# Performance work log

Measured on AMD Instinct MI355X. Metric: run time of the kernel, lower is better.

The kernel has to match this reference:

```python
import jax, jax.numpy as jnp
import numpy as np

B = 131072    # batch of toy 2D points
H = 256       # effective hidden width (dims[1], = out_dims * group_card)
NB = 8        # n_blocks i-ResBlocks
NMID = 3      # middle layers: dims 2->256->256->256->256->2 => 1 in + 3 mid + 1 out
NPS = 5       # n_power_series terms for log-det trace estimator


def setup_inputs() -> dict:
    key = jax.random.key(0)
    ks = jax.random.split(key, 8)
    # small scales keep each g-net contractive (coeff<1 Lipschitz, as spectral norm would)
    x  = jax.random.normal(ks[0], (B, 2), jnp.float32)
    v  = jax.random.normal(ks[1], (B, 2), jnp.float32)  # Hutchinson probe (n_samples=1)
    Wi = jax.random.normal(ks[2], (NB, 2, H), jnp.float32) * 0.05
    bi = jax.random.normal(ks[3], (NB, H), jnp.float32) * 0.01
    Wm = jax.random.normal(ks[4], (NB, NMID, H, H), jnp.float32) * (0.05 / np.sqrt(H))
    bm = jax.random.normal(ks[5], (NB, NMID, H), jnp.float32) * 0.01
    Wo = jax.random.normal(ks[6], (NB, H, 2), jnp.float32) * (0.05 / np.sqrt(H))
    bo = jax.random.normal(ks[7], (NB, 2), jnp.float32) * 0.01
    return {"x": x, "v": v, "Wi": Wi, "bi": bi, "Wm": Wm, "bm": bm, "Wo": Wo, "bo": bo}


def _g(x, Wi, bi, Wm, bm, Wo, bo):
    # equivariant 3x3 convs on 1x1 spatial maps == channel-mixing linears;
    # build_nnet appends the activation after EVERY conv, including the last.
    h = jax.nn.relu(x @ Wi + bi)
    for j in range(Wm.shape[0]):
        h = jax.nn.relu(h @ Wm[j] + bm[j])
    return jax.nn.relu(h @ Wo + bo)


def _iresblock(x, v, Wi, bi, Wm, bm, Wo, bo):
    gfun = lambda xx: _g(xx, Wi, bi, Wm, bm, Wo, bo)
    gx = gfun(x)
    # log det(I + J_g) ~= sum_{k=1..n} (-1)^{k+1}/k * v^T J_g^k v  (power series, Hutchinson)
    w = v
    logdet = jnp.zeros((x.shape[0], 1), x.dtype)
    for k in range(1, NPS + 1):
        _, w = jax.jvp(gfun, (x,), (w,))          # w <- J_g @ w
        coef = ((-1.0) ** (k + 1)) / k
        logdet = logdet + coef * jnp.sum(w * v, axis=1, keepdims=True)
    return x + gx, logdet


def reference(x, v, Wi, bi, Wm, bm, Wo, bo):
    z = x
    delta_logp = jnp.zeros((x.shape[0], 1), x.dtype)  # SequentialFlow: logpx - logdet per block
    for b in range(NB):
        z, ld = _iresblock(z, v, Wi[b], bi[b], Wm[b], bm[b], Wo[b], bo[b])
        delta_logp = delta_logp - ld
    return z, delta_logp
```

## Files before the change

### kernel.cpp

```cpp
#include <hip/hip_runtime.h>
#include <hip/hip_bf16.h>

#define BATCH 131072
#define H 256
#define NBLK 8
#define NMID 3
#define MS 32
#define RT_N 6
#define NT 512

typedef __attribute__((ext_vector_type(8))) short short8;
typedef __attribute__((ext_vector_type(4))) float f32x4;

__device__ __forceinline__ unsigned pk2(float a, float b) {
    unsigned ua = __float_as_uint(a) + 0x8000u;
    unsigned ub = __float_as_uint(b) + 0x8000u;
    return __builtin_amdgcn_perm(ub, ua, 0x07060302u);
}

__global__ void pack_w_kernel(const float* __restrict__ Wm, unsigned short* __restrict__ Wp) {
    int o = blockIdx.x * blockDim.x + threadIdx.x;
    if (o >= NBLK * NMID * 8192) return;
    int lane  = o & 63;
    int T     = (o >> 6) & 15;
    int kk    = (o >> 10) & 7;
    int layer = o >> 13;
    int n  = (T >> 2) * 64 + (lane & 15) * 4 + (T & 3);
    int k0 = kk * 32 + (lane >> 4) * 8;
    const float* src = Wm + (size_t)layer * H * H;
    unsigned int w[4];
    #pragma unroll
    for (int jj = 0; jj < 4; ++jj)
        w[jj] = pk2(src[(size_t)(k0 + 2*jj) * H + n], src[(size_t)(k0 + 2*jj + 1) * H + n]);
    uint4 val; val.x = w[0]; val.y = w[1]; val.z = w[2]; val.w = w[3];
    ((uint4*)Wp)[o] = val;
}

__device__ __forceinline__ void epilogue_write(const f32x4 (&acc)[3][4],
                                               const float* __restrict__ bias,
                                               unsigned short* __restrict__ Xs,
                                               int rg, int cg, int lane) {
    const int mcol = lane & 15, quad = lane >> 4;
    const int nb = cg * 64 + mcol * 4;
    const float4 bv = *(const float4*)(bias + nb);
    const int kkx = nb >> 5;
    const int qx  = (nb >> 3) & 3;
    const int jb  = nb & 7;
    const int kx1 = kkx & 1;
    #pragma unroll
    for (int r = 0; r < 4; ++r) {
        float pre[4], hv[4], ta[4], tb[4];
        pre[0] = acc[0][0][r] + bv.x; pre[1] = acc[0][1][r] + bv.y;
        pre[2] = acc[0][2][r] + bv.z; pre[3] = acc[0][3][r] + bv.w;
        #pragma unroll
        for (int c = 0; c < 4; ++c) {
            bool mk = pre[c] > 0.0f;
            hv[c] = mk ? pre[c]      : 0.0f;
            ta[c] = mk ? acc[1][c][r] : 0.0f;
            tb[c] = mk ? acc[2][c][r] : 0.0f;
        }
        int rowm = quad * 4 + r;
        int le   = qx * 16 + rowm;
        int scl  = (le ^ ((le >> 3) & 7)) ^ kx1;
        int e0   = (((rg * 8 + kkx) * 64 + scl) * 8) + jb;
        uint2 ph; ph.x = pk2(hv[0], hv[1]); ph.y = pk2(hv[2], hv[3]);
        uint2 pa; pa.x = pk2(ta[0], ta[1]); pa.y = pk2(ta[2], ta[3]);
        uint2 pb; pb.x = pk2(tb[0], tb[1]); pb.y = pk2(tb[2], tb[3]);
        *(uint2*)(Xs + e0)          = ph;
        *(uint2*)(Xs + e0 + 8192)   = pa;
        *(uint2*)(Xs + e0 + 16384)  = pb;
    }
}

__global__ __launch_bounds__(NT, 4)
void flow_kernel(const float* __restrict__ x, const float* __restrict__ v,
                 const float* __restrict__ Wi, const float* __restrict__ bi,
                 const float* __restrict__ bm, const float* __restrict__ Wo,
                 const float* __restrict__ bo,
                 const unsigned short* __restrict__ Wp,
                 float* __restrict__ out)
{
    __shared__ uint4 Xl4[RT_N * 8 * 64];
    __shared__ float zbuf[MS * 2];
    __shared__ float vbuf[MS * 2];

    unsigned short* Xs = (unsigned short*)Xl4;

    const int tid  = threadIdx.x;
    const int wave = tid >> 6;
    const int lane = tid & 63;
    const int mcol = lane & 15;
    const int quad = lane >> 4;
    const int rg   = wave >> 2;
    const int cg   = wave & 3;
    const int s0   = blockIdx.x * MS;
    const int rl   = lane ^ ((lane >> 3) & 7);

    float dlp = 0.0f;
    if (tid < MS) {
        zbuf[tid*2+0] = x[(size_t)(s0+tid)*2+0];
        zbuf[tid*2+1] = x[(size_t)(s0+tid)*2+1];
        vbuf[tid*2+0] = v[(size_t)(s0+tid)*2+0];
        vbuf[tid*2+1] = v[(size_t)(s0+tid)*2+1];
    }
    __syncthreads();

    for (int b = 0; b < NBLK; ++b) {
        if (tid < 384) {
            int rt = tid >> 6, cl = tid & 63;
            int l = cl ^ ((cl >> 3) & 7);
            int m = l & 15, q = l >> 4;
            int st = rt >> 1;
            uint4 pk = {0u, 0u, 0u, 0u};
            if (q == 0) {
                if (st == 0) {
                    int s = ((rt & 1) << 4) | m;
                    pk.x = pk2(zbuf[s*2+0], zbuf[s*2+1]);
                } else if (st == 1) pk.x = 0x00003F80u;
                else                pk.x = 0x3F800000u;
            }
            Xl4[rt * 512 + cl] = pk;
        }
        __syncthreads();

        const float* Wi0 = Wi + (size_t)b * 2 * H;
        const float* Wi1 = Wi0 + H;
        {
            short8 b0f[4];
            #pragma unroll
            for (int ct = 0; ct < 4; ++ct) {
                short8 z = {0,0,0,0,0,0,0,0};
                if (lane < 16) {
                    int n = cg * 64 + lane * 4 + ct;
                    unsigned p = pk2(Wi0[n], Wi1[n]);
                    z[0] = (short)(p & 0xFFFFu);
                    z[1] = (short)(p >> 16);
                }
                b0f[ct] = z;
            }
            f32x4 acc[3][4];
            #pragma unroll
            for (int st = 0; st < 3; ++st)
                #pragma unroll
                for (int ct = 0; ct < 4; ++ct)
                    acc[st][ct] = (f32x4){0.f, 0.f, 0.f, 0.f};
            #pragma unroll
            for (int st = 0; st < 3; ++st) {
                int rt = st * 2 + rg;
                short8 af = ((const short8*)Xl4)[(rt * 8) * 64 + rl];
                #pragma unroll
                for (int ct = 0; ct < 4; ++ct)
                    acc[st][ct] = __builtin_amdgcn_mfma_f32_16x16x32_bf16(af, b0f[ct], acc[st][ct], 0, 0, 0);
            }
            __syncthreads();
            epilogue_write(acc, bi + (size_t)b * H, Xs, rg, cg, lane);
            __syncthreads();
        }

        for (int li = 0; li < NMID; ++li) {
            const int layer = b * NMID + li;
            const short8* Bp  = ((const short8*)Wp) + (size_t)layer * 8192;
            const float* bias = bm + (size_t)layer * H;

            f32x4 acc[3][4];
            #pragma unroll
            for (int st = 0; st < 3; ++st)
                #pragma unroll
                for (int ct = 0; ct < 4; ++ct)
                    acc[st][ct] = (f32x4){0.f, 0.f, 0.f, 0.f};

            #pragma unroll 2
            for (int kk = 0; kk < 8; ++kk) {
                short8 bf[4];
                #pragma unroll
                for (int ct = 0; ct < 4; ++ct)
                    bf[ct] = Bp[(kk*16 + cg*4 + ct)*64 + lane];
                const int rls = rl ^ (kk & 1);
                #pragma unroll
                for (int st = 0; st < 3; ++st) {
                    int rt = st * 2 + rg;
                    short8 af = ((const short8*)Xl4)[(rt*8 + kk)*64 + rls];
                    #pragma unroll
                    for (int ct = 0; ct < 4; ++ct)
                        acc[st][ct] = __builtin_amdgcn_mfma_f32_16x16x32_bf16(af, bf[ct], acc[st][ct], 0, 0, 0);
                }
            }
            __syncthreads();
            epilogue_write(acc, bias, Xs, rg, cg, lane);
            __syncthreads();
        }

        const float* Wob = Wo + (size_t)b * H * 2;
        const float* bob = bo + (size_t)b * 2;
        {
            short8 b4 = {0,0,0,0,0,0,0,0};
            if (mcol < 2) {
                int kb = wave * 32 + quad * 8;
                #pragma unroll
                for (int jj = 0; jj < 4; ++jj) {
                    unsigned p = pk2(Wob[(kb + 2*jj) * 2 + mcol], Wob[(kb + 2*jj + 1) * 2 + mcol]);
                    b4[2*jj]   = (short)(p & 0xFFFFu);
                    b4[2*jj+1] = (short)(p >> 16);
                }
            }
            f32x4 accL[RT_N];
            #pragma unroll
            for (int rt = 0; rt < RT_N; ++rt) accL[rt] = (f32x4){0.f, 0.f, 0.f, 0.f};
            const int rls = rl ^ (wave & 1);
            #pragma unroll
            for (int rt = 0; rt < RT_N; ++rt) {
                short8 a0 = ((const short8*)Xl4)[(rt*8 + wave)*64 + rls];
                accL[rt] = __builtin_amdgcn_mfma_f32_16x16x32_bf16(a0, b4, accL[rt], 0, 0, 0);
            }
            __syncthreads();
            float* part = (float*)Xl4;
            if (mcol < 2) {
                #pragma unroll
                for (int rt = 0; rt < RT_N; ++rt)
                    #pragma unroll
                    for (int r = 0; r < 4; ++r)
                        part[((rt*16 + quad*4 + r)*2 + mcol)*8 + wave] = accL[rt][r];
            }
            __syncthreads();
            float* res = part + 1536;
            if (tid < 192) {
                float4 p4 = ((const float4*)part)[tid*2];
                float4 q4 = ((const float4*)part)[tid*2 + 1];
                res[tid] = (p4.x + p4.y + p4.z + p4.w) + (q4.x + q4.y + q4.z + q4.w);
            }
            __syncthreads();
            if (tid < MS) {
                int g = tid >> 4, row = tid & 15;
                int base = (g * 16 + row) * 2;
                float SH0 = res[base], SH1 = res[base + 1];
                float SA0 = res[base + 64], SA1 = res[base + 65];
                float SB0 = res[base + 128], SB1 = res[base + 129];
                float pre0 = SH0 + bob[0], pre1 = SH1 + bob[1];
                bool  m0 = pre0 > 0.f,     m1 = pre1 > 0.f;
                float gx0 = m0 ? pre0 : 0.f, gx1 = m1 ? pre1 : 0.f;
                float J00 = m0 ? SA0 : 0.f;
                float J01 = m0 ? SB0 : 0.f;
                float J10 = m1 ? SA1 : 0.f;
                float J11 = m1 ? SB1 : 0.f;
                float v0 = vbuf[tid*2+0], v1 = vbuf[tid*2+1];
                float w0 = v0, w1 = v1, ld = 0.f;
                const float coef[5] = {1.f, -0.5f, 1.f/3.f, -0.25f, 0.2f};
                #pragma unroll
                for (int k = 0; k < 5; ++k) {
                    float nw0 = fmaf(J00, w0, J01 * w1);
                    float nw1 = fmaf(J10, w0, J11 * w1);
                    w0 = nw0; w1 = nw1;
                    ld = fmaf(coef[k], fmaf(w0, v0, w1 * v1), ld);
                }
                zbuf[tid*2+0] += gx0;
                zbuf[tid*2+1] += gx1;
                dlp -= ld;
            }
        }
        __syncthreads();
    }

    if (tid < MS) {
        out[(size_t)(s0+tid)*2+0] = zbuf[tid*2+0];
        out[(size_t)(s0+tid)*2+1] = zbuf[tid*2+1];
        out[(size_t)2*BATCH + s0 + tid] = dlp;
    }
}

extern "C" void kernel_launch(void* const* d_in, const int* in_sizes, int n_in,
                              void* d_out, int out_size, void* d_ws, size_t ws_size,
                              hipStream_t stream) {
    const float* x  = (const float*)d_in[0];
    const float* v  = (const float*)d_in[1];
    const float* Wi = (const float*)d_in[2];
    const float* bi = (const float*)d_in[3];
    const float* Wm = (const float*)d_in[4];
    const float* bm = (const float*)d_in[5];
    const float* Wo = (const float*)d_in[6];
    const float* bo = (const float*)d_in[7];
    unsigned short* Wp = (unsigned short*)d_ws;

    int nchunks = NBLK * NMID * 8192;
    pack_w_kernel<<<(nchunks + 255) / 256, 256, 0, stream>>>(Wm, Wp);
    flow_kernel<<<BATCH / MS, NT, 0, stream>>>(x, v, Wi, bi, bm, Wo, bo, Wp, (float*)d_out);
}
```

Measured before the change: 1.190 ms.

## Halve samples per workgroup, fold bias into accumulator init, use hardware bf16 pack

Each workgroup now handles 16 samples with 256 threads instead of 32 samples with 512. Every wave computes all three stream tiles (h, tangent a, tangent b) for its 64-column slice, and the output layer splits K across waves as two k-steps each. The bias is loaded into the h accumulator before the MFMA loop, so the epilogue only applies ReLU masking, and packing now uses the v_cvt_pk_bf16_f32 instruction. Smaller blocks mean cheaper barriers and finer scheduling, but each sample's share of weight reads from L2 doubles because every block streams the full weight set. The packing instruction may also round differently from the old manual pack.

New measurement: 1.186 ms. About the same (-0.3%).

```diff
diff --git a/kernel.cpp b/kernel.cpp
--- a/kernel.cpp
+++ b/kernel.cpp
@@ -5,9 +5,9 @@
 #define H 256
 #define NBLK 8
 #define NMID 3
-#define MS 32
-#define RT_N 6
-#define NT 512
+#define MS 16
+#define RT_N 3
+#define NT 256
 
 typedef __attribute__((ext_vector_type(8))) short short8;
 typedef __attribute__((ext_vector_type(4))) float f32x4;
@@ -16,6 +16,11 @@
     unsigned ua = __float_as_uint(a) + 0x8000u;
     unsigned ub = __float_as_uint(b) + 0x8000u;
     return __builtin_amdgcn_perm(ub, ua, 0x07060302u);
+}
+__device__ __forceinline__ unsigned cpk(float a, float b) {
+    unsigned r;
+    asm("v_cvt_pk_bf16_f32 %0, %1, %2" : "=v"(r) : "v"(a), "v"(b));
+    return r;
 }
 
 __global__ void pack_w_kernel(const float* __restrict__ Wm, unsigned short* __restrict__ Wp) {
@@ -36,39 +41,35 @@
     ((uint4*)Wp)[o] = val;
 }
 
-__device__ __forceinline__ void epilogue_write(const f32x4 (&acc)[3][4],
-                                               const float* __restrict__ bias,
+__device__ __forceinline__ void epilogue_write(const f32x4 (&acc)[RT_N][4],
                                                unsigned short* __restrict__ Xs,
-                                               int rg, int cg, int lane) {
+                                               int cg, int lane) {
     const int mcol = lane & 15, quad = lane >> 4;
-    const int nb = cg * 64 + mcol * 4;
-    const float4 bv = *(const float4*)(bias + nb);
+    const int nb  = cg * 64 + mcol * 4;
     const int kkx = nb >> 5;
     const int qx  = (nb >> 3) & 3;
     const int jb  = nb & 7;
     const int kx1 = kkx & 1;
     #pragma unroll
     for (int r = 0; r < 4; ++r) {
-        float pre[4], hv[4], ta[4], tb[4];
-        pre[0] = acc[0][0][r] + bv.x; pre[1] = acc[0][1][r] + bv.y;
-        pre[2] = acc[0][2][r] + bv.z; pre[3] = acc[0][3][r] + bv.w;
+        float hv[4], ta[4], tb[4];
         #pragma unroll
         for (int c = 0; c < 4; ++c) {
-            bool mk = pre[c] > 0.0f;
-            hv[c] = mk ? pre[c]      : 0.0f;
+            float pre = acc[0][c][r];
+            bool mk = pre > 0.0f;
+            hv[c] = fmaxf(pre, 0.0f);
             ta[c] = mk ? acc[1][c][r] : 0.0f;
             tb[c] = mk ? acc[2][c][r] : 0.0f;
         }
-        int rowm = quad * 4 + r;
-        int le   = qx * 16 + rowm;
-        int scl  = (le ^ ((le >> 3) & 7)) ^ kx1;
-        int e0   = (((rg * 8 + kkx) * 64 + scl) * 8) + jb;
-        uint2 ph; ph.x = pk2(hv[0], hv[1]); ph.y = pk2(hv[2], hv[3]);
-        uint2 pa; pa.x = pk2(ta[0], ta[1]); pa.y = pk2(ta[2], ta[3]);
-        uint2 pb; pb.x = pk2(tb[0], tb[1]); pb.y = pk2(tb[2], tb[3]);
-        *(uint2*)(Xs + e0)          = ph;
-        *(uint2*)(Xs + e0 + 8192)   = pa;
-        *(uint2*)(Xs + e0 + 16384)  = pb;
+        int le  = qx * 16 + quad * 4 + r;
+        int scl = (le ^ ((le >> 3) & 7)) ^ kx1;
+        int e0  = ((kkx * 64 + scl) * 8) + jb;
+        uint2 ph; ph.x = cpk(hv[0], hv[1]); ph.y = cpk(hv[2], hv[3]);
+        uint2 pa; pa.x = cpk(ta[0], ta[1]); pa.y = cpk(ta[2], ta[3]);
+        uint2 pb; pb.x = cpk(tb[0], tb[1]); pb.y = cpk(tb[2], tb[3]);
+        *(uint2*)(Xs + e0)         = ph;
+        *(uint2*)(Xs + e0 + 4096)  = pa;
+        *(uint2*)(Xs + e0 + 8192)  = pb;
     }
 }
 
@@ -87,12 +88,10 @@
     unsigned short* Xs = (unsigned short*)Xl4;
 
     const int tid  = threadIdx.x;
-    const int wave = tid >> 6;
+    const int cg   = tid >> 6;
     const int lane = tid & 63;
     const int mcol = lane & 15;
     const int quad = lane >> 4;
-    const int rg   = wave >> 2;
-    const int cg   = wave & 3;
     const int s0   = blockIdx.x * MS;
     const int rl   = lane ^ ((lane >> 3) & 7);
 
@@ -106,20 +105,17 @@
     __syncthreads();
 
     for (int b = 0; b < NBLK; ++b) {
-        if (tid < 384) {
-            int rt = tid >> 6, cl = tid & 63;
+        if (tid < 192) {
+            int st = tid >> 6, cl = tid & 63;
             int l = cl ^ ((cl >> 3) & 7);
             int m = l & 15, q = l >> 4;
-            int st = rt >> 1;
             uint4 pk = {0u, 0u, 0u, 0u};
             if (q == 0) {
-                if (st == 0) {
-                    int s = ((rt & 1) << 4) | m;
-                    pk.x = pk2(zbuf[s*2+0], zbuf[s*2+1]);
-                } else if (st == 1) pk.x = 0x00003F80u;
-                else                pk.x = 0x3F800000u;
-            }
-            Xl4[rt * 512 + cl] = pk;
+                if (st == 0)      pk.x = pk2(zbuf[m*2+0], zbuf[m*2+1]);
+                else if (st == 1) pk.x = 0x00003F80u;
+                else              pk.x = 0x3F800000u;
+            }
+            Xl4[st * 512 + cl] = pk;
         }
         __syncthreads();
 
@@ -138,22 +134,24 @@
                 }
                 b0f[ct] = z;
             }
-            f32x4 acc[3][4];
-            #pragma unroll
-            for (int st = 0; st < 3; ++st)
-                #pragma unroll
-                for (int ct = 0; ct < 4; ++ct)
-                    acc[st][ct] = (f32x4){0.f, 0.f, 0.f, 0.f};
-            #pragma unroll
-            for (int st = 0; st < 3; ++st) {
-                int rt = st * 2 + rg;
-                short8 af = ((const short8*)Xl4)[(rt * 8) * 64 + rl];
+            const float4 bv = *(const float4*)(bi + (size_t)b * H + cg * 64 + mcol * 4);
+            f32x4 acc[RT_N][4];
+            #pragma unroll
+            for (int ct = 0; ct < 4; ++ct) {
+                float bb = (ct == 0) ? bv.x : (ct == 1) ? bv.y : (ct == 2) ? bv.z : bv.w;
+                acc[0][ct] = (f32x4){bb, bb, bb, bb};
+                acc[1][ct] = (f32x4){0.f, 0.f, 0.f, 0.f};
+                acc[2][ct] = (f32x4){0.f, 0.f, 0.f, 0.f};
+            }
+            #pragma unroll
+            for (int st = 0; st < RT_N; ++st) {
+                short8 af = ((const short8*)Xl4)[(st * 8) * 64 + rl];
                 #pragma unroll
                 for (int ct = 0; ct < 4; ++ct)
                     acc[st][ct] = __builtin_amdgcn_mfma_f32_16x16x32_bf16(af, b0f[ct], acc[st][ct], 0, 0, 0);
             }
             __syncthreads();
-            epilogue_write(acc, bi + (size_t)b * H, Xs, rg, cg, lane);
+            epilogue_write(acc, Xs, cg, lane);
             __syncthreads();
         }
 
@@ -162,12 +160,15 @@
             const short8* Bp  = ((const short8*)Wp) + (size_t)layer * 8192;
             const float* bias = bm + (size_t)layer * H;
 
-            f32x4 acc[3][4];
-            #pragma unroll
-            for (int st = 0; st < 3; ++st)
-                #pragma unroll
-                for (int ct = 0; ct < 4; ++ct)
-                    acc[st][ct] = (f32x4){0.f, 0.f, 0.f, 0.f};
+            const float4 bv = *(const float4*)(bias + cg * 64 + mcol * 4);
+            f32x4 acc[RT_N][4];
+            #pragma unroll
+            for (int ct = 0; ct < 4; ++ct) {
+                float bb = (ct == 0) ? bv.x : (ct == 1) ? bv.y : (ct == 2) ? bv.z : bv.w;
+                acc[0][ct] = (f32x4){bb, bb, bb, bb};
+                acc[1][ct] = (f32x4){0.f, 0.f, 0.f, 0.f};
+                acc[2][ct] = (f32x4){0.f, 0.f, 0.f, 0.f};
+            }
 
             #pragma unroll 2
             for (int kk = 0; kk < 8; ++kk) {
@@ -177,64 +178,69 @@
                     bf[ct] = Bp[(kk*16 + cg*4 + ct)*64 + lane];
                 const int rls = rl ^ (kk & 1);
                 #pragma unroll
-                for (int st = 0; st < 3; ++st) {
-                    int rt = st * 2 + rg;
-                    short8 af = ((const short8*)Xl4)[(rt*8 + kk)*64 + rls];
+                for (int st = 0; st < RT_N; ++st) {
+                    short8 af = ((const short8*)Xl4)[(st*8 + kk)*64 + rls];
                     #pragma unroll
                     for (int ct = 0; ct < 4; ++ct)
                         acc[st][ct] = __builtin_amdgcn_mfma_f32_16x16x32_bf16(af, bf[ct], acc[st][ct], 0, 0, 0);
                 }
             }
             __syncthreads();
-            epilogue_write(acc, bias, Xs, rg, cg, lane);
+            epilogue_write(acc, Xs, cg, lane);
             __syncthreads();
         }
 
         const float* Wob = Wo + (size_t)b * H * 2;
         const float* bob = bo + (size_t)b * 2;
         {
-            short8 b4 = {0,0,0,0,0,0,0,0};
-            if (mcol < 2) {
-                int kb = wave * 32 + quad * 8;
-                #pragma unroll
-                for (int jj = 0; jj < 4; ++jj) {
-                    unsigned p = pk2(Wob[(kb + 2*jj) * 2 + mcol], Wob[(kb + 2*jj + 1) * 2 + mcol]);
-                    b4[2*jj]   = (short)(p & 0xFFFFu);
-                    b4[2*jj+1] = (short)(p >> 16);
-                }
+            short8 b4[2];
+            #pragma unroll
+            for (int kki = 0; kki < 2; ++kki) {
+                short8 z = {0,0,0,0,0,0,0,0};
+                if (mcol < 2) {
+                    int kb = (cg * 2 + kki) * 32 + quad * 8;
+                    #pragma unroll
+                    for (int jj = 0; jj < 4; ++jj) {
+                        unsigned p = pk2(Wob[(kb + 2*jj) * 2 + mcol], Wob[(kb + 2*jj + 1) * 2 + mcol]);
+                        z[2*jj]   = (short)(p & 0xFFFFu);
+                        z[2*jj+1] = (short)(p >> 16);
+                    }
+                }
+                b4[kki] = z;
             }
             f32x4 accL[RT_N];
             #pragma unroll
-            for (int rt = 0; rt < RT_N; ++rt) accL[rt] = (f32x4){0.f, 0.f, 0.f, 0.f};
-            const int rls = rl ^ (wave & 1);
-            #pragma unroll
-            for (int rt = 0; rt < RT_N; ++rt) {
-                short8 a0 = ((const short8*)Xl4)[(rt*8 + wave)*64 + rls];
-                accL[rt] = __builtin_amdgcn_mfma_f32_16x16x32_bf16(a0, b4, accL[rt], 0, 0, 0);
+            for (int st = 0; st < RT_N; ++st) accL[st] = (f32x4){0.f, 0.f, 0.f, 0.f};
+            #pragma unroll
+            for (int kki = 0; kki < 2; ++kki) {
+                const int rls = rl ^ (kki & 1);
+                #pragma unroll
+                for (int st = 0; st < RT_N; ++st) {
+                    short8 a0 = ((const short8*)Xl4)[(st*8 + cg*2 + kki)*64 + rls];
+                    accL[st] = __builtin_amdgcn_mfma_f32_16x16x32_bf16(a0, b4[kki], accL[st], 0, 0, 0);
+                }
             }
             __syncthreads();
             float* part = (float*)Xl4;
             if (mcol < 2) {
                 #pragma unroll
-                for (int rt = 0; rt < RT_N; ++rt)
+                for (int st = 0; st < RT_N; ++st)
                     #pragma unroll
                     for (int r = 0; r < 4; ++r)
-                        part[((rt*16 + quad*4 + r)*2 + mcol)*8 + wave] = accL[rt][r];
-            }
-            __syncthreads();
-            float* res = part + 1536;
-            if (tid < 192) {
-                float4 p4 = ((const float4*)part)[tid*2];
-                float4 q4 = ((const float4*)part)[tid*2 + 1];
-                res[tid] = (p4.x + p4.y + p4.z + p4.w) + (q4.x + q4.y + q4.z + q4.w);
+                        part[((st*16 + quad*4 + r)*2 + mcol)*4 + cg] = accL[st][r];
+            }
+            __syncthreads();
+            float* res = part + 384;
+            if (tid < 96) {
+                float4 p4 = ((const float4*)part)[tid];
+                res[tid] = p4.x + p4.y + p4.z + p4.w;
             }
             __syncthreads();
             if (tid < MS) {
-                int g = tid >> 4, row = tid & 15;
-                int base = (g * 16 + row) * 2;
-                float SH0 = res[base], SH1 = res[base + 1];
-                float SA0 = res[base + 64], SA1 = res[base + 65];
-                float SB0 = res[base + 128], SB1 = res[base + 129];
+                int base = tid * 2;
+                float SH0 = res[base],      SH1 = res[base + 1];
+                float SA0 = res[base + 32], SA1 = res[base + 33];
+                float SB0 = res[base + 64], SB1 = res[base + 65];
                 float pre0 = SH0 + bob[0], pre1 = SH1 + bob[1];
                 bool  m0 = pre0 > 0.f,     m1 = pre1 > 0.f;
                 float gx0 = m0 ? pre0 : 0.f, gx1 = m1 ? pre1 : 0.f;
```
